# Optimization experiments

Hardware: AMD Instinct MI355X
Metric: run time of the kernel (lower is better)

Reference implementation:

```python
import jax, jax.numpy as jnp
import numpy as np

EMBED = 1024
D_MODEL = 1024
HEADS = 16
HEAD_DIM = D_MODEL // HEADS


def setup_inputs() -> dict:
    key = jax.random.key(0)
    ks = jax.random.split(key, 9)
    s = 1.0 / np.sqrt(EMBED)
    inp = {
        "x": jax.random.normal(ks[0], (4, 2048, EMBED), dtype=jnp.float32),
        "Wq": jax.random.uniform(ks[1], (EMBED, D_MODEL), jnp.float32, -s, s),
        "bq": jax.random.uniform(ks[2], (D_MODEL,), jnp.float32, -s, s),
        "Wk": jax.random.uniform(ks[3], (EMBED, D_MODEL), jnp.float32, -s, s),
        "bk": jax.random.uniform(ks[4], (D_MODEL,), jnp.float32, -s, s),
        "Wv": jax.random.uniform(ks[5], (EMBED, D_MODEL), jnp.float32, -s, s),
        "bv": jax.random.uniform(ks[6], (D_MODEL,), jnp.float32, -s, s),
        "Wo": jax.random.uniform(ks[7], (D_MODEL, D_MODEL), jnp.float32, -s, s),
        "bo": jax.random.uniform(ks[8], (D_MODEL,), jnp.float32, -s, s),
    }
    return inp


def reference(x, Wq, bq, Wk, bk, Wv, bv, Wo, bo):
    B, S, _ = x.shape
    # projections -> [B, H, S, Dh]
    def proj(W, b):
        return (x @ W + b).reshape(B, S, HEADS, HEAD_DIM).transpose(0, 2, 1, 3)
    q = proj(Wq, bq)
    k = proj(Wk, bk)
    v = proj(Wv, bv)
    energy = jnp.einsum("bhqd,bhkd->bhqk", q, k)  # [B,H,S,S]
    attn = jax.nn.softmax(energy / jnp.sqrt(jnp.float32(HEAD_DIM)), axis=-1)
    out = jnp.einsum("bhqk,bhkd->bhqd", attn, v)
    out = out.transpose(0, 2, 1, 3).reshape(B, S, D_MODEL)
    return out @ Wo + bo
```

## Files before the change

kernel.cpp:

```cpp
#include <hip/hip_runtime.h>

typedef unsigned short u16;
typedef unsigned int u32;
typedef unsigned short u16x8 __attribute__((ext_vector_type(8)));
typedef unsigned int u32x4 __attribute__((ext_vector_type(4)));
typedef __bf16 bf16x8 __attribute__((ext_vector_type(8)));
typedef float f32x4 __attribute__((ext_vector_type(4)));

#define QSCALE 0.18033688011112042f

__device__ __forceinline__ u16 f2bf(float f) {
    unsigned u = __float_as_uint(f);
    u += 0x7fffu + ((u >> 16) & 1u);
    return (u16)(u >> 16);
}

__device__ __forceinline__ u32 cvtpk(float lo, float hi) {
    u32 r;
    asm("v_cvt_pk_bf16_f32 %0, %1, %2" : "=v"(r) : "v"(lo), "v"(hi));
    return r;
}

__device__ __forceinline__ bf16x8 ldfrag(const u16* p) {
    return __builtin_bit_cast(bf16x8, *(const u16x8*)p);
}

__device__ __forceinline__ void async_cp16(const void* g, void* l) {
    __builtin_amdgcn_global_load_lds(
        (const __attribute__((address_space(1))) unsigned int*)g,
        (__attribute__((address_space(3))) unsigned int*)l, 16, 0, 0);
}

__device__ __forceinline__ uint2 pack4(float a, float b, float c, float d) {
    uint2 w;
    w.x = (u32)f2bf(a) | ((u32)f2bf(b) << 16);
    w.y = (u32)f2bf(c) | ((u32)f2bf(d) << 16);
    return w;
}

__device__ __forceinline__ f32x4 mfma32(bf16x8 a, bf16x8 b, f32x4 c) {
    return __builtin_amdgcn_mfma_f32_16x16x32_bf16(a, b, c, 0, 0, 0);
}


__global__ void cvt_x(const float* __restrict__ x, u16* __restrict__ xb, int n4) {
    int i = blockIdx.x * blockDim.x + threadIdx.x;
    if (i < n4) {
        float4 v = ((const float4*)x)[i];
        ushort4 o;
        o.x = f2bf(v.x); o.y = f2bf(v.y); o.z = f2bf(v.z); o.w = f2bf(v.w);
        ((ushort4*)xb)[i] = o;
    }
}

__global__ __launch_bounds__(1024) void transp(const float* __restrict__ src, u16* __restrict__ dst) {
    __shared__ float t[32][33];
    int bx = blockIdx.x * 32, by = blockIdx.y * 32;
    t[threadIdx.y][threadIdx.x] = src[(by + threadIdx.y) * 1024 + bx + threadIdx.x];
    __syncthreads();
    dst[(bx + threadIdx.y) * 1024 + by + threadIdx.x] = f2bf(t[threadIdx.x][threadIdx.y]);
}

__global__ void mkbias(const float* __restrict__ bq, const float* __restrict__ bk,
                       const float* __restrict__ bv, float* __restrict__ bqkv) {
    int i = blockIdx.x * blockDim.x + threadIdx.x;
    if (i < 3072) bqkv[i] = (i < 1024) ? bq[i] : (i < 2048 ? bk[i - 1024] : bv[i - 2048]);
}


template <int EPI>
__global__ __launch_bounds__(256)
void gemm128(const u16* __restrict__ A, const u16* __restrict__ Bt,
             const float* __restrict__ bias,
             u16* __restrict__ Qb, u16* __restrict__ Kb, u16* __restrict__ Vt,
             float* __restrict__ outf) {
    __shared__ u16 Asm[128 * 64];
    __shared__ u16 Bsm[128 * 64];
    int tid = threadIdx.x;
    int wave = tid >> 6, lane = tid & 63;
    int lr = lane & 15, lq = lane >> 4;
    int wrow = (wave >> 1) * 64, wcol = (wave & 1) * 64;
    int tileM = blockIdx.y * 128, tileN = blockIdx.x * 128;

    f32x4 acc[4][4];
    for (int i = 0; i < 4; i++)
        for (int j = 0; j < 4; j++)
            acc[i][j] = (f32x4){0.f, 0.f, 0.f, 0.f};

    int srow = tid >> 3;
    int sg = (tid & 7) ^ (srow & 7);
    const u16* ga = A + (tileM + srow) * 1024 + sg * 8;
    const u16* gb = Bt + (tileN + srow) * 1024 + sg * 8;
    u16* la = &Asm[tid * 8];
    u16* lb = &Bsm[tid * 8];

    int sw0 = ((lq ^ (lr & 7)) << 3);
    int sw1 = (((4 + lq) ^ (lr & 7)) << 3);

    for (int k0 = 0; k0 < 1024; k0 += 64) {
        for (int rnd = 0; rnd < 4; rnd++) {
            async_cp16(ga + k0 + rnd * 32 * 1024, la + rnd * 2048);
            async_cp16(gb + k0 + rnd * 32 * 1024, lb + rnd * 2048);
        }
        __syncthreads();
        for (int ko = 0; ko < 2; ko++) {
            int sw = ko ? sw1 : sw0;
            bf16x8 af[4], bfr[4];
            for (int mt = 0; mt < 4; mt++) af[mt] = ldfrag(&Asm[(wrow + mt * 16 + lr) * 64 + sw]);
            for (int nt = 0; nt < 4; nt++) bfr[nt] = ldfrag(&Bsm[(wcol + nt * 16 + lr) * 64 + sw]);
            for (int mt = 0; mt < 4; mt++)
                for (int nt = 0; nt < 4; nt++) {
                    if (EPI == 1)
                        acc[mt][nt] = __builtin_amdgcn_mfma_f32_16x16x32_bf16(af[mt], bfr[nt], acc[mt][nt], 0, 0, 0);
                    else
                        acc[mt][nt] = __builtin_amdgcn_mfma_f32_16x16x32_bf16(bfr[nt], af[mt], acc[mt][nt], 0, 0, 0);
                }
        }
        __syncthreads();
    }

    if (EPI == 0) {
        for (int mt = 0; mt < 4; mt++) {
            int m = tileM + wrow + mt * 16 + lr;
            int b = m >> 11, s = m & 2047;
            for (int nt = 0; nt < 4; nt++) {
                int n0 = tileN + wcol + nt * 16 + lq * 4;
                float4 bn = *(const float4*)&bias[n0];
                int which = n0 >> 10, d = n0 & 1023, h = d >> 6, dh = d & 63;
                u16* dst = (which ? Kb : Qb) + ((b * 16 + h) * 2048 + s) * 64 + dh;
                f32x4 v = acc[mt][nt];
                uint2 w;
                if (which == 0)
                    w = pack4((v[0] + bn.x) * QSCALE, (v[1] + bn.y) * QSCALE,
                              (v[2] + bn.z) * QSCALE, (v[3] + bn.w) * QSCALE);
                else
                    w = pack4(v[0] + bn.x, v[1] + bn.y, v[2] + bn.z, v[3] + bn.w);
                *(uint2*)dst = w;
            }
        }
    } else if (EPI == 1) {
        for (int nt = 0; nt < 4; nt++) {
            int n0 = tileN + wcol + nt * 16 + lr;
            float bn = bias[n0];
            int h = n0 >> 6, dh = n0 & 63;
            for (int mt = 0; mt < 4; mt++) {
                int m0 = tileM + wrow + mt * 16 + lq * 4;
                int b = m0 >> 11, s = m0 & 2047;
                f32x4 v = acc[mt][nt];
                uint2 w = pack4(v[0] + bn, v[1] + bn, v[2] + bn, v[3] + bn);
                *(uint2*)(Vt + ((b * 16 + h) * 64 + dh) * 2048 + s) = w;
            }
        }
    } else {
        for (int mt = 0; mt < 4; mt++) {
            int m = tileM + wrow + mt * 16 + lr;
            for (int nt = 0; nt < 4; nt++) {
                int n0 = tileN + wcol + nt * 16 + lq * 4;
                float4 bn = *(const float4*)&bias[n0];
                f32x4 v = acc[mt][nt];
                float4 st = {v[0] + bn.x, v[1] + bn.y, v[2] + bn.z, v[3] + bn.w};
                *(float4*)&outf[m * 1024 + n0] = st;
            }
        }
    }
}

__global__ __launch_bounds__(256)
void attn(const u16* __restrict__ Qb, const u16* __restrict__ Kb,
          const u16* __restrict__ Vt, u16* __restrict__ Ob) {
    __shared__ u16 Ksm[2][64 * 64];
    __shared__ u16 Vsm[2][64 * 64];
    int tid = threadIdx.x;
    int wave = tid >> 6, lane = tid & 63;
    int lr = lane & 15, lq = lane >> 4;
    int bh = blockIdx.y;
    int b = bh >> 4, h = bh & 15;
    int qbase = blockIdx.x * 128 + wave * 32;

    const u16* Qh = Qb + bh * 2048 * 64;
    const u16* Kh = Kb + bh * 2048 * 64;
    const u16* Vh = Vt + bh * 64 * 2048;

    bf16x8 qf[2][2];
    for (int s = 0; s < 2; s++)
        for (int hf = 0; hf < 2; hf++)
            qf[s][hf] = ldfrag(Qh + (qbase + s * 16 + lr) * 64 + hf * 32 + lq * 8);

    f32x4 o[2][4];
    float lacc[2] = {0.f, 0.f};
    for (int s = 0; s < 2; s++)
        for (int dt = 0; dt < 4; dt++) o[s][dt] = (f32x4){0.f, 0.f, 0.f, 0.f};

    int row0 = ((lr & 12) << 1) | (lr & 3);
    int gg = (lr & 3) | (((lr >> 2) & 1) << 2);
    int kofs = row0 * 64 + ((lq ^ gg) << 3);
    int vofs0 = (lq ^ (lr & 7)) << 3;

    int sr = tid >> 3, sg = tid & 7;
    int gK = (sg ^ ((sr & 3) | (((sr >> 3) & 1) << 2))) << 3;
    int gV = (sg ^ (sr & 7)) << 3;
    const u16* gk = Kh + sr * 64 + gK;
    const u16* gv = Vh + sr * 2048 + gV;

    async_cp16(gk, &Ksm[0][tid * 8]);
    async_cp16(gk + 32 * 64, &Ksm[0][tid * 8 + 32 * 64]);
    async_cp16(gv, &Vsm[0][tid * 8]);
    async_cp16(gv + 32 * 2048, &Vsm[0][tid * 8 + 32 * 64]);

    for (int it = 0; it < 32; ++it) {
        int p = it & 1;
        __syncthreads();

        if (it < 31) {
            gk += 64 * 64; gv += 64;
            async_cp16(gk, &Ksm[p ^ 1][tid * 8]);
            async_cp16(gk + 32 * 64, &Ksm[p ^ 1][tid * 8 + 32 * 64]);
            async_cp16(gv, &Vsm[p ^ 1][tid * 8]);
            async_cp16(gv + 32 * 2048, &Vsm[p ^ 1][tid * 8 + 32 * 64]);
        }

        const u16* Kp = Ksm[p];
        const u16* Vp = Vsm[p];

        bf16x8 pb[2][2];
        for (int kg2 = 0; kg2 < 2; kg2++) {
            int ka = kofs + kg2 * 2048;
            bf16x8 kA0 = ldfrag(Kp + ka);
            bf16x8 kA1 = ldfrag(Kp + (ka ^ 32));
            bf16x8 kB0 = ldfrag(Kp + ka + 256);
            bf16x8 kB1 = ldfrag(Kp + ((ka + 256) ^ 32));
            for (int s = 0; s < 2; s++) {
                f32x4 sa = (f32x4){0.f, 0.f, 0.f, 0.f};
                f32x4 sb = (f32x4){0.f, 0.f, 0.f, 0.f};
                sa = mfma32(kA0, qf[s][0], sa);
                sa = mfma32(kA1, qf[s][1], sa);
                sb = mfma32(kB0, qf[s][0], sb);
                sb = mfma32(kB1, qf[s][1], sb);
                float e0 = __builtin_amdgcn_exp2f(sa[0]);
                float e1 = __builtin_amdgcn_exp2f(sa[1]);
                float e2 = __builtin_amdgcn_exp2f(sa[2]);
                float e3 = __builtin_amdgcn_exp2f(sa[3]);
                float e4 = __builtin_amdgcn_exp2f(sb[0]);
                float e5 = __builtin_amdgcn_exp2f(sb[1]);
                float e6 = __builtin_amdgcn_exp2f(sb[2]);
                float e7 = __builtin_amdgcn_exp2f(sb[3]);
                lacc[s] += ((e0 + e1) + (e2 + e3)) + ((e4 + e5) + (e6 + e7));
                u32x4 pw = {cvtpk(e0, e1), cvtpk(e2, e3), cvtpk(e4, e5), cvtpk(e6, e7)};
                pb[kg2][s] = __builtin_bit_cast(bf16x8, pw);
            }
        }

        for (int dt = 0; dt < 4; dt++) {
            int rb = (dt * 16 + lr) * 64;
            bf16x8 v0 = ldfrag(Vp + rb + vofs0);
            bf16x8 v1 = ldfrag(Vp + rb + (vofs0 ^ 32));
            o[0][dt] = mfma32(v0, pb[0][0], o[0][dt]);
            o[1][dt] = mfma32(v0, pb[0][1], o[1][dt]);
            o[0][dt] = mfma32(v1, pb[1][0], o[0][dt]);
            o[1][dt] = mfma32(v1, pb[1][1], o[1][dt]);
        }
    }

    for (int s = 0; s < 2; s++) {
        lacc[s] += __shfl_xor(lacc[s], 16);
        lacc[s] += __shfl_xor(lacc[s], 32);
    }

    for (int s = 0; s < 2; s++) {
        float linv = 1.0f / lacc[s];
        int q = qbase + s * 16 + lr;
        u16* obase = Ob + (b * 2048 + q) * 1024 + h * 64 + lq * 4;
        for (int dt = 0; dt < 4; dt++) {
            uint2 w = pack4(o[s][dt][0] * linv, o[s][dt][1] * linv,
                            o[s][dt][2] * linv, o[s][dt][3] * linv);
            *(uint2*)(obase + dt * 16) = w;
        }
    }
}


extern "C" void kernel_launch(void* const* d_in, const int* in_sizes, int n_in,
                              void* d_out, int out_size, void* d_ws, size_t ws_size,
                              hipStream_t stream) {
    const float* x  = (const float*)d_in[0];
    const float* Wq = (const float*)d_in[1];
    const float* bq = (const float*)d_in[2];
    const float* Wk = (const float*)d_in[3];
    const float* bk = (const float*)d_in[4];
    const float* Wv = (const float*)d_in[5];
    const float* bv = (const float*)d_in[6];
    const float* Wo = (const float*)d_in[7];
    const float* bo = (const float*)d_in[8];
    float* out = (float*)d_out;

    char* ws = (char*)d_ws;
    u16* xb    = (u16*)ws;
    u16* Wt    = (u16*)(ws + (16u << 20));
    u16* Wot   = (u16*)(ws + (22u << 20));
    float* bqkv = (float*)(ws + (24u << 20));
    u16* Vtb   = (u16*)(ws + (25u << 20));
    u16* Qb    = (u16*)d_out;
    u16* Kb    = Qb + 4 * 16 * 2048 * 64;

    cvt_x<<<8192, 256, 0, stream>>>(x, xb, 8192 * 1024 / 4);
    dim3 tb(32, 32);
    transp<<<dim3(32, 32), tb, 0, stream>>>(Wq, Wt);
    transp<<<dim3(32, 32), tb, 0, stream>>>(Wk, Wt + 1024 * 1024);
    transp<<<dim3(32, 32), tb, 0, stream>>>(Wv, Wt + 2 * 1024 * 1024);
    transp<<<dim3(32, 32), tb, 0, stream>>>(Wo, Wot);
    mkbias<<<12, 256, 0, stream>>>(bq, bk, bv, bqkv);

    gemm128<0><<<dim3(16, 64), 256, 0, stream>>>(xb, Wt, bqkv, Qb, Kb, nullptr, nullptr);
    gemm128<1><<<dim3(8, 64), 256, 0, stream>>>(xb, Wt + 2048 * 1024, bqkv + 2048,
                                                nullptr, nullptr, Vtb, nullptr);
    attn<<<dim3(16, 64), 256, 0, stream>>>(Qb, Kb, Vtb, xb);
    gemm128<2><<<dim3(8, 64), 256, 0, stream>>>(xb, Wot, bo, nullptr, nullptr, nullptr, out);
}
```

Before: 307.4 us.

## Use 256x128 GEMM tiles with triple-buffered async LDS pipeline

```diff
diff --git a/kernel.cpp b/kernel.cpp
--- a/kernel.cpp
+++ b/kernel.cpp
@@ -69,61 +69,103 @@
 
 
 template <int EPI>
-__global__ __launch_bounds__(256)
-void gemm128(const u16* __restrict__ A, const u16* __restrict__ Bt,
+__global__ __launch_bounds__(512)
+void gemm256(const u16* __restrict__ A, const u16* __restrict__ Bt,
              const float* __restrict__ bias,
              u16* __restrict__ Qb, u16* __restrict__ Kb, u16* __restrict__ Vt,
              float* __restrict__ outf) {
-    __shared__ u16 Asm[128 * 64];
-    __shared__ u16 Bsm[128 * 64];
+    __shared__ u16 Asm3[3][256 * 64];
+    __shared__ u16 Bsm3[3][128 * 64];
+
     int tid = threadIdx.x;
     int wave = tid >> 6, lane = tid & 63;
     int lr = lane & 15, lq = lane >> 4;
     int wrow = (wave >> 1) * 64, wcol = (wave & 1) * 64;
-    int tileM = blockIdx.y * 128, tileN = blockIdx.x * 128;
+    int tileM = blockIdx.y * 256, tileN = blockIdx.x * 128;
 
     f32x4 acc[4][4];
+#pragma unroll
     for (int i = 0; i < 4; i++)
+#pragma unroll
         for (int j = 0; j < 4; j++)
             acc[i][j] = (f32x4){0.f, 0.f, 0.f, 0.f};
 
     int srow = tid >> 3;
-    int sg = (tid & 7) ^ (srow & 7);
-    const u16* ga = A + (tileM + srow) * 1024 + sg * 8;
-    const u16* gb = Bt + (tileN + srow) * 1024 + sg * 8;
-    u16* la = &Asm[tid * 8];
-    u16* lb = &Bsm[tid * 8];
-
-    int sw0 = ((lq ^ (lr & 7)) << 3);
-    int sw1 = (((4 + lq) ^ (lr & 7)) << 3);
-
-    for (int k0 = 0; k0 < 1024; k0 += 64) {
-        for (int rnd = 0; rnd < 4; rnd++) {
-            async_cp16(ga + k0 + rnd * 32 * 1024, la + rnd * 2048);
-            async_cp16(gb + k0 + rnd * 32 * 1024, lb + rnd * 2048);
-        }
-        __syncthreads();
-        for (int ko = 0; ko < 2; ko++) {
-            int sw = ko ? sw1 : sw0;
-            bf16x8 af[4], bfr[4];
-            for (int mt = 0; mt < 4; mt++) af[mt] = ldfrag(&Asm[(wrow + mt * 16 + lr) * 64 + sw]);
-            for (int nt = 0; nt < 4; nt++) bfr[nt] = ldfrag(&Bsm[(wcol + nt * 16 + lr) * 64 + sw]);
-            for (int mt = 0; mt < 4; mt++)
-                for (int nt = 0; nt < 4; nt++) {
+    int sgrp = (tid & 7) ^ (srow & 7);
+    const u16* gA = A + (tileM + srow) * 1024 + sgrp * 8;
+    const u16* gB = Bt + (tileN + srow) * 1024 + sgrp * 8;
+
+#define STAGE(buf, kc)                                                        \
+    do {                                                                      \
+        _Pragma("unroll")                                                     \
+        for (int r = 0; r < 4; ++r)                                           \
+            async_cp16(gA + (kc) + r * 64 * 1024, &Asm3[buf][tid * 8 + r * 4096]); \
+        _Pragma("unroll")                                                     \
+        for (int r = 0; r < 2; ++r)                                           \
+            async_cp16(gB + (kc) + r * 64 * 1024, &Bsm3[buf][tid * 8 + r * 4096]); \
+    } while (0)
+
+    STAGE(0, 0);
+    STAGE(1, 64);
+    asm volatile("s_waitcnt vmcnt(6)" ::: "memory");
+    __builtin_amdgcn_s_barrier();
+
+    for (int t = 0; t < 16; ++t) {
+        int cur = t % 3;
+        STAGE((t + 2) % 3, ((t + 2) & 15) * 64);
+
+        const u16* Ap = &Asm3[cur][0];
+        const u16* Bp = &Bsm3[cur][0];
+        bf16x8 af[4][2], bfr[2][2];
+#pragma unroll
+        for (int mt = 0; mt < 4; ++mt)
+#pragma unroll
+            for (int ko = 0; ko < 2; ++ko)
+                af[mt][ko] = ldfrag(&Ap[(wrow + mt * 16 + lr) * 64 +
+                                        (((ko * 4 + lq) ^ (lr & 7)) << 3)]);
+#pragma unroll
+        for (int nt = 0; nt < 2; ++nt)
+#pragma unroll
+            for (int ko = 0; ko < 2; ++ko)
+                bfr[nt][ko] = ldfrag(&Bp[(wcol + nt * 16 + lr) * 64 +
+                                         (((ko * 4 + lq) ^ (lr & 7)) << 3)]);
+        bf16x8 bfr2[2][2];
+#pragma unroll
+        for (int nt = 0; nt < 2; ++nt)
+#pragma unroll
+            for (int ko = 0; ko < 2; ++ko)
+                bfr2[nt][ko] = ldfrag(&Bp[(wcol + (nt + 2) * 16 + lr) * 64 +
+                                          (((ko * 4 + lq) ^ (lr & 7)) << 3)]);
+
+        asm volatile("s_waitcnt lgkmcnt(0)" ::: "memory");
+        __builtin_amdgcn_sched_barrier(0);
+        __builtin_amdgcn_s_setprio(1);
+#pragma unroll
+        for (int ko = 0; ko < 2; ++ko)
+#pragma unroll
+            for (int mt = 0; mt < 4; ++mt)
+#pragma unroll
+                for (int nt = 0; nt < 4; ++nt) {
+                    bf16x8 b = (nt < 2) ? bfr[nt][ko] : bfr2[nt - 2][ko];
                     if (EPI == 1)
-                        acc[mt][nt] = __builtin_amdgcn_mfma_f32_16x16x32_bf16(af[mt], bfr[nt], acc[mt][nt], 0, 0, 0);
+                        acc[mt][nt] = mfma32(af[mt][ko], b, acc[mt][nt]);
                     else
-                        acc[mt][nt] = __builtin_amdgcn_mfma_f32_16x16x32_bf16(bfr[nt], af[mt], acc[mt][nt], 0, 0, 0);
+                        acc[mt][nt] = mfma32(b, af[mt][ko], acc[mt][nt]);
                 }
-        }
-        __syncthreads();
-    }
+        __builtin_amdgcn_s_setprio(0);
+        asm volatile("s_waitcnt vmcnt(6)" ::: "memory");
+        __builtin_amdgcn_s_barrier();
+    }
+    asm volatile("s_waitcnt vmcnt(0)" ::: "memory");
+#undef STAGE
 
     if (EPI == 0) {
-        for (int mt = 0; mt < 4; mt++) {
+#pragma unroll
+        for (int mt = 0; mt < 4; ++mt) {
             int m = tileM + wrow + mt * 16 + lr;
             int b = m >> 11, s = m & 2047;
-            for (int nt = 0; nt < 4; nt++) {
+#pragma unroll
+            for (int nt = 0; nt < 4; ++nt) {
                 int n0 = tileN + wcol + nt * 16 + lq * 4;
                 float4 bn = *(const float4*)&bias[n0];
                 int which = n0 >> 10, d = n0 & 1023, h = d >> 6, dh = d & 63;
@@ -139,11 +181,13 @@
             }
         }
     } else if (EPI == 1) {
-        for (int nt = 0; nt < 4; nt++) {
+#pragma unroll
+        for (int nt = 0; nt < 4; ++nt) {
             int n0 = tileN + wcol + nt * 16 + lr;
             float bn = bias[n0];
             int h = n0 >> 6, dh = n0 & 63;
-            for (int mt = 0; mt < 4; mt++) {
+#pragma unroll
+            for (int mt = 0; mt < 4; ++mt) {
                 int m0 = tileM + wrow + mt * 16 + lq * 4;
                 int b = m0 >> 11, s = m0 & 2047;
                 f32x4 v = acc[mt][nt];
@@ -152,9 +196,11 @@
             }
         }
     } else {
-        for (int mt = 0; mt < 4; mt++) {
+#pragma unroll
+        for (int mt = 0; mt < 4; ++mt) {
             int m = tileM + wrow + mt * 16 + lr;
-            for (int nt = 0; nt < 4; nt++) {
+#pragma unroll
+            for (int nt = 0; nt < 4; ++nt) {
                 int n0 = tileN + wcol + nt * 16 + lq * 4;
                 float4 bn = *(const float4*)&bias[n0];
                 f32x4 v = acc[mt][nt];
@@ -310,9 +356,9 @@
     transp<<<dim3(32, 32), tb, 0, stream>>>(Wo, Wot);
     mkbias<<<12, 256, 0, stream>>>(bq, bk, bv, bqkv);
 
-    gemm128<0><<<dim3(16, 64), 256, 0, stream>>>(xb, Wt, bqkv, Qb, Kb, nullptr, nullptr);
-    gemm128<1><<<dim3(8, 64), 256, 0, stream>>>(xb, Wt + 2048 * 1024, bqkv + 2048,
+    gemm256<0><<<dim3(16, 32), 512, 0, stream>>>(xb, Wt, bqkv, Qb, Kb, nullptr, nullptr);
+    gemm256<1><<<dim3(8, 32), 512, 0, stream>>>(xb, Wt + 2048 * 1024, bqkv + 2048,
                                                 nullptr, nullptr, Vtb, nullptr);
     attn<<<dim3(16, 64), 256, 0, stream>>>(Qb, Kb, Vtb, xb);
-    gemm128<2><<<dim3(8, 64), 256, 0, stream>>>(xb, Wot, bo, nullptr, nullptr, nullptr, out);
-}
+    gemm256<2><<<dim3(8, 32), 512, 0, stream>>>(xb, Wot, bo, nullptr, nullptr, nullptr, out);
+}
```

Measured after the change: 316.9 us. 1.03x slower.
